# Optimization experiments

Measured on AMD Instinct MI355X. Metric: run time of the kernel, lower is better.

## Reference

```python
import jax, jax.numpy as jnp
import numpy as np

B, T, V, E, H = 512, 512, 50000, 100, 40


def gru_dir(x, lens, Wih, Whh, bih, bhh, reverse):
    """One GRU direction with length masking (PyTorch gate math).
    x: [B,T,I]; returns (out [B,T,H] zero-padded past lens, h_last [B,H])."""
    Bx, Tx, _ = x.shape
    Hh = Whh.shape[1]
    # precompute input-side gates: [T,B,3H]
    gx = jnp.einsum('bti,gi->tbg', x, Wih) + bih
    valid = (jnp.arange(Tx)[:, None] < lens[None, :])[..., None]  # [T,B,1]

    def step(h, inputs):
        gx_t, v = inputs
        gh = h @ Whh.T + bhh
        r = jax.nn.sigmoid(gx_t[:, :Hh] + gh[:, :Hh])
        z = jax.nn.sigmoid(gx_t[:, Hh:2 * Hh] + gh[:, Hh:2 * Hh])
        n = jnp.tanh(gx_t[:, 2 * Hh:] + r * gh[:, 2 * Hh:])
        hn = (1.0 - z) * n + z * h
        h = jnp.where(v, hn, h)          # freeze state past valid length
        return h, jnp.where(v, hn, 0.0)  # pad_packed_sequence zero-fills

    h0 = jnp.zeros((Bx, Hh), x.dtype)
    h_last, outs = jax.lax.scan(step, h0, (gx, valid), reverse=reverse)
    return jnp.transpose(outs, (1, 0, 2)), h_last


def setup_inputs() -> dict:
    key = jax.random.key(0)
    ks = jax.random.split(key, 24)
    text_len = jax.random.randint(ks[0], (B,), 1, T + 1)
    text = jax.random.randint(ks[1], (B, T), 1, V)
    text = jnp.where(jnp.arange(T)[None, :] < text_len[:, None], text, 0)
    s = 0.1
    emb = jax.random.normal(ks[2], (V, E), jnp.float32) * s
    emb = emb.at[0].set(0.0)  # padding_idx=0
    def mk(k, shape):
        return jax.random.normal(k, shape, jnp.float32) * s
    inp = {
        'text': text, 'text_len': text_len, 'emb': emb,
        'Wih0f': mk(ks[3], (3 * H, E)), 'Whh0f': mk(ks[4], (3 * H, H)),
        'bih0f': mk(ks[5], (3 * H,)), 'bhh0f': mk(ks[6], (3 * H,)),
        'Wih0b': mk(ks[7], (3 * H, E)), 'Whh0b': mk(ks[8], (3 * H, H)),
        'bih0b': mk(ks[9], (3 * H,)), 'bhh0b': mk(ks[10], (3 * H,)),
        'Wih1f': mk(ks[11], (3 * H, 2 * H)), 'Whh1f': mk(ks[12], (3 * H, H)),
        'bih1f': mk(ks[13], (3 * H,)), 'bhh1f': mk(ks[14], (3 * H,)),
        'Wih1b': mk(ks[15], (3 * H, 2 * H)), 'Whh1b': mk(ks[16], (3 * H, H)),
        'bih1b': mk(ks[17], (3 * H,)), 'bhh1b': mk(ks[18], (3 * H,)),
        'fc1_W': mk(ks[19], (128, 8 * H)), 'fc1_b': mk(ks[20], (128,)),
        'fc2_W': mk(ks[21], (1, 128)), 'fc2_b': mk(ks[22], (1,)),
    }
    return inp


def forward(text, text_len, emb, Wih0f, Whh0f, bih0f, bhh0f, Wih0b, Whh0b, bih0b, bhh0b,
            Wih1f, Whh1f, bih1f, bhh1f, Wih1b, Whh1b, bih1b, bhh1b,
            fc1_W, fc1_b, fc2_W, fc2_b):
    x = emb[text]  # [B,T,E]
    # layer 0 (bidirectional)
    of0, hf0 = gru_dir(x, text_len, Wih0f, Whh0f, bih0f, bhh0f, False)
    ob0, hb0 = gru_dir(x, text_len, Wih0b, Whh0b, bih0b, bhh0b, True)
    x1 = jnp.concatenate([of0, ob0], axis=-1)  # [B,T,2H]; inter-layer dropout is eval no-op
    # layer 1 (bidirectional)
    of1, hf1 = gru_dir(x1, text_len, Wih1f, Whh1f, bih1f, bhh1f, False)
    ob1, hb1 = gru_dir(x1, text_len, Wih1b, Whh1b, bih1b, bhh1b, True)
    out = jnp.concatenate([of1, ob1], axis=-1)  # [B,T,2H], zero past lens
    # masked avg / max pooling over valid timesteps
    avg_pool = jnp.sum(out, axis=1) / text_len[:, None].astype(out.dtype)
    valid = (jnp.arange(T)[None, :] < text_len[:, None])[..., None]  # [B,T,1]
    max_pool = jnp.max(jnp.where(valid, out, -jnp.inf), axis=1)
    # hidden order: [l0_fwd, l0_bwd, l1_fwd, l1_bwd]; cat([-1],[-2],[-3],[-4],...)
    pool_cat = jnp.concatenate([hb1, hf1, hb0, hf0, avg_pool, max_pool], axis=1)  # [B,8H]
    h = pool_cat @ fc1_W.T + fc1_b
    h = jnp.where(h >= 0, h, 0.01 * h)  # leaky_relu (dropouts are eval no-ops)
    return h @ fc2_W.T + fc2_b  # [B,1]


def reference(text, text_len, emb, Wih0f, Whh0f, bih0f, bhh0f, Wih0b, Whh0b, bih0b, bhh0b,
              Wih1f, Whh1f, bih1f, bhh1f, Wih1b, Whh1b, bih1b, bhh1b,
              fc1_W, fc1_b, fc2_W, fc2_b):
    return forward(text, text_len, emb, Wih0f, Whh0f, bih0f, bhh0f, Wih0b, Whh0b, bih0b, bhh0b,
                   Wih1f, Whh1f, bih1f, bhh1f, Wih1b, Whh1b, bih1b, bhh1b,
                   fc1_W, fc1_b, fc2_W, fc2_b)
```

## Files before the change

### kernel.cpp

```cpp
#include <hip/hip_runtime.h>
#include <hip/hip_fp16.h>

#define BB 512
#define TT 512
#define EE 100
#define HH 40
#define GG 120
#define TC 256
#define NC 2
#define NT (TC/64)
#define X1S 96
#define GXS 160

typedef _Float16 h2_t __attribute__((ext_vector_type(2)));
typedef _Float16 h8_t __attribute__((ext_vector_type(8)));
typedef float    f4_t __attribute__((ext_vector_type(4)));

__device__ __forceinline__ float fdot2_(h2_t a, h2_t b, float c) {
    return __builtin_amdgcn_fdot2(a, b, c, false);
}
__device__ __forceinline__ h2_t pack2_(float x, float y) {
    h2_t r; r[0] = (_Float16)x; r[1] = (_Float16)y; return r;
}
__device__ __forceinline__ float sigmoid_(float x) {
    return __builtin_amdgcn_rcpf(1.0f + __expf(-x));
}
__device__ __forceinline__ float tanhfast_(float x) {
    return 1.0f - 2.0f * __builtin_amdgcn_rcpf(__expf(2.0f * x) + 1.0f);
}

template<int K, bool GATHER>
__global__ __launch_bounds__(256, 1) void fused_kernel(
    const int cg, const int cs, const int nScan,
    const int* __restrict__ text, const __half* __restrict__ emb16,
    const __half* __restrict__ Xh,
    const _Float16* __restrict__ Wt,
    const float* __restrict__ bf, const float* __restrict__ bb,
    __half* __restrict__ gxW, const __half* __restrict__ gxR,
    const _Float16* __restrict__ WhhL,
    const float* __restrict__ bhhF, const float* __restrict__ bhhB,
    const int* __restrict__ lens,
    __half* __restrict__ out0,
    float* __restrict__ hcar, float* __restrict__ hlast,
    float* __restrict__ sumb, float* __restrict__ maxb)
{
    constexpr int KS = (K == 100) ? 4 : 3;
    const int tid = threadIdx.x;

    if ((int)blockIdx.x < nScan) {
        __builtin_amdgcn_s_setprio(3);
        const int wave = tid >> 6, j = tid & 63;
        if (j >= HH) return;
        const int chain = blockIdx.x * 4 + wave;
        const int dir = chain >> 9;
        const int b   = chain & (BB - 1);
        const float* bhh = dir ? bhhB : bhhF;

        h8_t R0,R1,R2,R3,R4, Z0,Z1,Z2,Z3,Z4, N0,N1,N2,N3,N4;
        {
            const _Float16* wr = WhhL + (size_t)dir * 4800;
            const h8_t* pr = (const h8_t*)(wr + (size_t)j * 40);
            const h8_t* pz = (const h8_t*)(wr + (size_t)(40 + j) * 40);
            const h8_t* pn = (const h8_t*)(wr + (size_t)(80 + j) * 40);
            R0=pr[0]; R1=pr[1]; R2=pr[2]; R3=pr[3]; R4=pr[4];
            Z0=pz[0]; Z1=pz[1]; Z2=pz[2]; Z3=pz[3]; Z4=pz[4];
            N0=pn[0]; N1=pn[1]; N2=pn[2]; N3=pn[3]; N4=pn[4];
        }
        asm volatile("" : "+v"(R0),"+v"(R1),"+v"(R2),"+v"(R3),"+v"(R4),
                          "+v"(Z0),"+v"(Z1),"+v"(Z2),"+v"(Z3),"+v"(Z4),
                          "+v"(N0),"+v"(N1),"+v"(N2),"+v"(N3),"+v"(N4));
        const float br = bhh[j], bz = bhh[HH + j], bn = bhh[2*HH + j];
        const int len = lens[b];
        const int chunk = dir ? (NC - 1 - cs) : cs;
        const int tbase = chunk * TC;

        int sBeg, sEnd;
        if (dir == 0) { sBeg = 0; sEnd = min(TC, max(0, len - tbase)); }
        else          { sBeg = max(0, tbase + TC - len); sEnd = TC; }

        float h = (cs == 0) ? 0.0f : hcar[(size_t)(dir * BB + b) * HH + j];
        float psum = 0.0f, pmax = -3.4e38f;
        const size_t gxRow = ((size_t)dir * BB + b) * TC;

        h2_t H0{},H1{},H2{},H3{},H4{},H5{},H6{},H7{},H8{},H9{},
             H10{},H11{},H12{},H13{},H14{},H15{},H16{},H17{},H18{},H19{};
#define RDL(L) __builtin_bit_cast(h2_t, __builtin_amdgcn_readlane(pk_, (L)))
#define REFRESH_H(val) do { \
        const int v_ = (int)__builtin_bit_cast(unsigned short, (_Float16)(val)); \
        const int t_ = __builtin_amdgcn_update_dpp(0, v_, 0x101, 0xf, 0xf, true); \
        const int pk_ = (t_ << 16) | (v_ & 0xffff); \
        H0=RDL(0);  H1=RDL(2);  H2=RDL(4);  H3=RDL(6);  H4=RDL(8); \
        H5=RDL(10); H6=RDL(12); H7=RDL(14); H8=RDL(16); H9=RDL(18); \
        H10=RDL(20); H11=RDL(22); H12=RDL(24); H13=RDL(26); H14=RDL(28); \
        H15=RDL(30); H16=RDL(32); H17=RDL(34); H18=RDL(36); H19=RDL(38); \
} while (0)
        REFRESH_H(h);

        struct G3 { __half r, z, n; };
        auto ldg3 = [&](int sc) -> G3 {
            const int scc = max(0, min(sc, sEnd - 1));
            const int tl = dir ? (TC - 1 - scc) : scc;
            const uint2 v = *(const uint2*)(gxR + (gxRow + tl) * GXS + j * 4);
            G3 g;
            g.r = __builtin_bit_cast(__half, (unsigned short)(v.x & 0xffff));
            g.z = __builtin_bit_cast(__half, (unsigned short)(v.x >> 16));
            g.n = __builtin_bit_cast(__half, (unsigned short)(v.y & 0xffff));
            return g;
        };
#define SL(V,i) __builtin_shufflevector(V, V, 2*(i), 2*(i)+1)
#define DOTQ(Rq,Zq,Nq, A,B,C,D) \
        r0 = fdot2_(SL(Rq,0), (A), r0); \
        z0 = fdot2_(SL(Zq,0), (A), z0); \
        n0 = fdot2_(SL(Nq,0), (A), n0); \
        r1 = fdot2_(SL(Rq,1), (B), r1); \
        z1 = fdot2_(SL(Zq,1), (B), z1); \
        n1 = fdot2_(SL(Nq,1), (B), n1); \
        r0 = fdot2_(SL(Rq,2), (C), r0); \
        z0 = fdot2_(SL(Zq,2), (C), z0); \
        n0 = fdot2_(SL(Nq,2), (C), n0); \
        r1 = fdot2_(SL(Rq,3), (D), r1); \
        z1 = fdot2_(SL(Zq,3), (D), z1); \
        n1 = fdot2_(SL(Nq,3), (D), n1);

        constexpr int PF = 4;
        auto step = [&](int s, G3& g, bool pf) {
            G3 nx;
            if (pf) nx = ldg3(s + PF);
            const int tloc = dir ? (TC - 1 - s) : s;
            float r0 = br, r1 = 0.f, z0 = bz, z1 = 0.f, n0 = bn, n1 = 0.f;
            DOTQ(R0,Z0,N0, H0,H1,H2,H3)
            DOTQ(R1,Z1,N1, H4,H5,H6,H7)
            DOTQ(R2,Z2,N2, H8,H9,H10,H11)
            DOTQ(R3,Z3,N3, H12,H13,H14,H15)
            DOTQ(R4,Z4,N4, H16,H17,H18,H19)
            const float rr = sigmoid_(__half2float(g.r) + r0 + r1);
            const float zz = sigmoid_(__half2float(g.z) + z0 + z1);
            const float nn = tanhfast_(__half2float(g.n) + rr * (n0 + n1));
            const float hn = (1.0f - zz) * nn + zz * h;
            h = hn;
            REFRESH_H(hn);
            if (GATHER) {
                const int t = tbase + tloc;
                out0[((size_t)b * TT + t) * X1S + dir*HH + j] = __float2half(hn);
            } else {
                psum += hn;
                pmax = fmaxf(pmax, hn);
            }
            if (pf) g = nx;
        };

        G3 q0 = {}, q1 = {}, q2 = {}, q3 = {};
        if (sBeg < sEnd) {
            q0 = ldg3(sBeg);
            q1 = ldg3(sBeg + 1);
            q2 = ldg3(sBeg + 2);
            q3 = ldg3(sBeg + 3);
        }
        int s = sBeg;
        for (; s + PF <= sEnd; s += PF) {
            step(s + 0, q0, true);
            step(s + 1, q1, true);
            step(s + 2, q2, true);
            step(s + 3, q3, true);
        }
        if (s     < sEnd) step(s,     q0, false);
        if (s + 1 < sEnd) step(s + 1, q1, false);
        if (s + 2 < sEnd) step(s + 2, q2, false);

        hcar[(size_t)(dir * BB + b) * HH + j] = h;
        const int layer = GATHER ? 0 : 1;
        if (cs == NC - 1)
            hlast[((size_t)(layer * 2 + dir) * BB + b) * HH + j] = h;
        if (!GATHER) {
            const size_t pi = (size_t)b * (2*HH) + dir*HH + j;
            if (cs == 0) { sumb[pi] = psum;  maxb[pi] = pmax; }
            else         { sumb[pi] += psum; maxb[pi] = fmaxf(maxb[pi], pmax); }
        }
        return;
    }

    __builtin_amdgcn_s_setprio(0);
    const int gid = blockIdx.x - nScan;
    const int b    = gid & (BB - 1);
    const int tile = (gid >> 9) & (NT - 1);
    const int dir  = gid >> (9 + 2);
    const int chunk = dir ? (NC - 1 - cg) : cg;
    const int tbase = chunk * TC + tile * 64;
    if (tbase >= lens[b]) return;
    const float* bias = dir ? bb : bf;
    const _Float16* Wg = Wt + (size_t)dir * (KS * 8 * 64 * 8);

    const int w = tid >> 6, l = tid & 63;
    const int row = l & 15, kq = l >> 4;
    const int t0 = tbase + w * 16 + row;
    h8_t A[4];
    if (GATHER) {
        const int tok = text[b * TT + t0];
        const _Float16* ap = (const _Float16*)emb16 + (size_t)tok * 128 + kq * 8;
        #pragma unroll
        for (int ks = 0; ks < KS; ++ks) A[ks] = *(const h8_t*)(ap + ks * 32);
    } else {
        const _Float16* ap = (const _Float16*)Xh + ((size_t)b * TT + t0) * X1S + kq * 8;
        #pragma unroll
        for (int ks = 0; ks < KS; ++ks) A[ks] = *(const h8_t*)(ap + ks * 32);
    }

    f4_t acc[8] = {};
    #pragma unroll
    for (int ks = 0; ks < KS; ++ks)
        #pragma unroll
        for (int f = 0; f < 8; ++f) {
            const h8_t Bf = *(const h8_t*)(Wg + ((size_t)(ks * 8 + f) * 64 + l) * 8);
            acc[f] = __builtin_amdgcn_mfma_f32_16x16x32_f16(A[ks], Bf, acc[f], 0, 0, 0);
        }

    const size_t rowB = ((size_t)dir * BB + b) * TC;
    const int gb = l & 15, rq = l >> 4;
    #pragma unroll
    for (int f = 0; f < 8; ++f) {
        const int gate = f * 16 + gb;
        if (gate < GG) {
            const int jj   = (gate >= 80) ? (gate - 80) : (gate >= 40 ? gate - 40 : gate);
            const int slot = (gate >= 80) ? 2 : (gate >= 40 ? 1 : 0);
            const float bv = bias[gate];
            #pragma unroll
            for (int r = 0; r < 4; ++r) {
                const int tloc = tile * 64 + w * 16 + rq * 4 + r;
                gxW[(rowB + tloc) * GXS + jj * 4 + slot] = __float2half(acc[f][r] + bv);
            }
        }
    }
}

#define NE2 (50000 * 64)
#define NW0 (2*4*8*64)
#define NW1 (2*3*8*64)
#define NHH (4*120*20)
#define NP0 (BB*TT*8)
__global__ __launch_bounds__(256) void prep_kernel(
    const float* __restrict__ emb,
    const float* __restrict__ Wih0f, const float* __restrict__ Wih0b,
    const float* __restrict__ Wih1f, const float* __restrict__ Wih1b,
    const float* __restrict__ Whh0f, const float* __restrict__ Whh0b,
    const float* __restrict__ Whh1f, const float* __restrict__ Whh1b,
    __half* __restrict__ emb16, _Float16* __restrict__ Wt16,
    _Float16* __restrict__ Whh16, __half* __restrict__ out0)
{
    const int gid = blockIdx.x * 256 + threadIdx.x;
    if (gid < NE2) {
        const int v = gid >> 6, q2 = gid & 63;
        const int k0 = q2 * 2;
        float x0 = 0.f, x1 = 0.f;
        if (k0 < EE) { x0 = emb[(size_t)v * EE + k0]; x1 = emb[(size_t)v * EE + k0 + 1]; }
        ((h2_t*)emb16)[(size_t)v * 64 + q2] = pack2_(x0, x1);
        return;
    }
    int e = gid - NE2;
    if (e < NP0) {
        const int row = e >> 3, q = e & 7;
        ((h2_t*)out0)[(size_t)row * 48 + 40 + q] = pack2_(0.f, 0.f);
        return;
    }
    e -= NP0;
    if (e < NW0) {
        const int l = e & 63, f = (e >> 6) & 7, ks = (e >> 9) & 3, dir = e >> 11;
        const float* W = dir ? Wih0b : Wih0f;
        const int col = f * 16 + (l & 15);
        const int kb  = ks * 32 + (l >> 4) * 8;
        _Float16* dst = Wt16 + (size_t)e * 8;
        #pragma unroll
        for (int i = 0; i < 8; ++i) {
            const int k = kb + i;
            dst[i] = (_Float16)((col < GG && k < EE) ? W[(size_t)col * EE + k] : 0.f);
        }
        return;
    }
    e -= NW0;
    if (e < NW1) {
        const int l = e & 63, f = (e >> 6) & 7;
        const int t = e >> 9;
        const int ks = t % 3, dir = t / 3;
        const float* W = dir ? Wih1b : Wih1f;
        const int col = f * 16 + (l & 15);
        const int kb  = ks * 32 + (l >> 4) * 8;
        _Float16* dst = Wt16 + (size_t)(NW0 + e) * 8;
        #pragma unroll
        for (int i = 0; i < 8; ++i) {
            const int k = kb + i;
            dst[i] = (_Float16)((col < GG && k < 2*HH) ? W[(size_t)col * (2*HH) + k] : 0.f);
        }
        return;
    }
    e -= NW1;
    if (e < NHH) {
        const int ld = e / 2400, rem = e - ld * 2400;
        const int row2 = rem / 20, kk = rem - row2 * 20;
        const float* W = (ld == 0) ? Whh0f : (ld == 1) ? Whh0b
                       : (ld == 2) ? Whh1f : Whh1b;
        ((h2_t*)Whh16)[e] = pack2_(W[row2*HH + 2*kk], W[row2*HH + 2*kk + 1]);
    }
}

__global__ __launch_bounds__(128) void fc_kernel(
    const float* __restrict__ hlast, const float* __restrict__ sumb,
    const float* __restrict__ maxb, const int* __restrict__ lens,
    const float* __restrict__ fc1W, const float* __restrict__ fc1b,
    const float* __restrict__ fc2W, const float* __restrict__ fc2b,
    float* __restrict__ out)
{
    __shared__ float pool[8 * HH];
    __shared__ float red[128];
    const int b = blockIdx.x, tid = threadIdx.x;
    if (tid < HH) {
        pool[tid]        = hlast[(size_t)(3*BB + b) * HH + tid];
        pool[HH + tid]   = hlast[(size_t)(2*BB + b) * HH + tid];
        pool[2*HH + tid] = hlast[(size_t)(1*BB + b) * HH + tid];
        pool[3*HH + tid] = hlast[(size_t)(0*BB + b) * HH + tid];
    }
    const float invLen = 1.0f / (float)lens[b];
    if (tid < 2*HH) {
        pool[4*HH + tid] = sumb[(size_t)b * 2*HH + tid] * invLen;
        pool[6*HH + tid] = maxb[(size_t)b * 2*HH + tid];
    }
    __syncthreads();
    float acc = fc1b[tid];
    for (int k = 0; k < 8*HH; ++k)
        acc = fmaf(pool[k], fc1W[(size_t)tid * (8*HH) + k], acc);
    float v = (acc >= 0.0f) ? acc : 0.01f * acc;
    red[tid] = v * fc2W[tid];
    __syncthreads();
    for (int s = 64; s > 0; s >>= 1) {
        if (tid < s) red[tid] += red[tid + s];
        __syncthreads();
    }
    if (tid == 0) out[b] = red[0] + fc2b[0];
}

extern "C" void kernel_launch(void* const* d_in, const int* in_sizes, int n_in,
                              void* d_out, int out_size, void* d_ws, size_t ws_size,
                              hipStream_t stream) {
    const int*   text  = (const int*)d_in[0];
    const int*   lens  = (const int*)d_in[1];
    const float* emb   = (const float*)d_in[2];
    const float* Wih0f = (const float*)d_in[3];
    const float* Whh0f = (const float*)d_in[4];
    const float* bih0f = (const float*)d_in[5];
    const float* bhh0f = (const float*)d_in[6];
    const float* Wih0b = (const float*)d_in[7];
    const float* Whh0b = (const float*)d_in[8];
    const float* bih0b = (const float*)d_in[9];
    const float* bhh0b = (const float*)d_in[10];
    const float* Wih1f = (const float*)d_in[11];
    const float* Whh1f = (const float*)d_in[12];
    const float* bih1f = (const float*)d_in[13];
    const float* bhh1f = (const float*)d_in[14];
    const float* Wih1b = (const float*)d_in[15];
    const float* Whh1b = (const float*)d_in[16];
    const float* bih1b = (const float*)d_in[17];
    const float* bhh1b = (const float*)d_in[18];
    const float* fc1W  = (const float*)d_in[19];
    const float* fc1b  = (const float*)d_in[20];
    const float* fc2W  = (const float*)d_in[21];
    const float* fc2b  = (const float*)d_in[22];
    float* out = (float*)d_out;

    char* p = (char*)d_ws;
    const size_t gxB = (size_t)2 * BB * TC * GXS * sizeof(__half);
    __half* gxb0  = (__half*)p;  p += gxB;
    __half* gxb1  = (__half*)p;  p += gxB;
    __half* out0  = (__half*)p;  p += (size_t)BB * TT * X1S * sizeof(__half);
    float*  hcar  = (float*)p;   p += (size_t)2 * BB * HH * sizeof(float);
    float*  hlast = (float*)p;   p += (size_t)4 * BB * HH * sizeof(float);
    float*  sumb  = (float*)p;   p += (size_t)BB * 2 * HH * sizeof(float);
    float*  maxb  = (float*)p;   p += (size_t)BB * 2 * HH * sizeof(float);
    __half*    emb16 = (__half*)p;    p += (size_t)50000 * 128 * sizeof(__half);
    _Float16*  Wt16  = (_Float16*)p;  p += (size_t)(NW0 + NW1) * 8 * sizeof(_Float16);
    _Float16*  Whh16 = (_Float16*)p;
    __half* gxb[2] = { gxb0, gxb1 };

    const int NG = BB * 2 * NT;
    const int NS = 256;

    {
        const int total = NE2 + NP0 + NW0 + NW1 + NHH;
        prep_kernel<<<(total + 255) / 256, 256, 0, stream>>>(
            emb, Wih0f, Wih0b, Wih1f, Wih1b, Whh0f, Whh0b, Whh1f, Whh1b,
            emb16, Wt16, Whh16, out0);
    }

    fused_kernel<EE, true><<<NG, 256, 0, stream>>>(0, 0, 0,
        text, emb16, nullptr, Wt16, bih0f, bih0b,
        gxb[0], gxb[0], Whh16, bhh0f, bhh0b,
        lens, out0, hcar, hlast, sumb, maxb);
    for (int ci = 1; ci < NC; ++ci)
        fused_kernel<EE, true><<<NS + NG, 256, 0, stream>>>(ci, ci - 1, NS,
            text, emb16, nullptr, Wt16, bih0f, bih0b,
            gxb[ci & 1], gxb[(ci - 1) & 1], Whh16, bhh0f, bhh0b,
            lens, out0, hcar, hlast, sumb, maxb);
    fused_kernel<EE, true><<<NS, 256, 0, stream>>>(0, NC - 1, NS,
        text, emb16, nullptr, Wt16, bih0f, bih0b,
        gxb[0], gxb[(NC - 1) & 1], Whh16, bhh0f, bhh0b,
        lens, out0, hcar, hlast, sumb, maxb);

    fused_kernel<2*HH, false><<<NG, 256, 0, stream>>>(0, 0, 0,
        text, emb16, out0, Wt16 + (size_t)NW0 * 8, bih1f, bih1b,
        gxb[0], gxb[0], Whh16 + 9600, bhh1f, bhh1b,
        lens, out0, hcar, hlast, sumb, maxb);
    for (int ci = 1; ci < NC; ++ci)
        fused_kernel<2*HH, false><<<NS + NG, 256, 0, stream>>>(ci, ci - 1, NS,
            text, emb16, out0, Wt16 + (size_t)NW0 * 8, bih1f, bih1b,
            gxb[ci & 1], gxb[(ci - 1) & 1], Whh16 + 9600, bhh1f, bhh1b,
            lens, out0, hcar, hlast, sumb, maxb);
    fused_kernel<2*HH, false><<<NS, 256, 0, stream>>>(0, NC - 1, NS,
        text, emb16, out0, Wt16 + (size_t)NW0 * 8, bih1f, bih1b,
        gxb[0], gxb[(NC - 1) & 1], Whh16 + 9600, bhh1f, bhh1b,
        lens, out0, hcar, hlast, sumb, maxb);

    fc_kernel<<<BB, 128, 0, stream>>>(hlast, sumb, maxb, lens,
        fc1W, fc1b, fc2W, fc2b, out);
}
```

Before: 506.3 us.

## Double-buffer input-gate loads in 16-step windows for the GRU scan

Replaces the rolling 4-step register prefetch of precomputed input gates with two 16-entry register buffers. The next 16-step window is loaded while the current one is processed. The aim is to hide global-memory latency behind the serial recurrence by issuing many loads in a batch. The extra buffers raise VGPR pressure, and the per-step bounds checks inside the unrolled windows add branching at partial windows.

```diff
diff --git a/kernel.cpp b/kernel.cpp
--- a/kernel.cpp
+++ b/kernel.cpp
@@ -96,17 +96,6 @@
 } while (0)
         REFRESH_H(h);
 
-        struct G3 { __half r, z, n; };
-        auto ldg3 = [&](int sc) -> G3 {
-            const int scc = max(0, min(sc, sEnd - 1));
-            const int tl = dir ? (TC - 1 - scc) : scc;
-            const uint2 v = *(const uint2*)(gxR + (gxRow + tl) * GXS + j * 4);
-            G3 g;
-            g.r = __builtin_bit_cast(__half, (unsigned short)(v.x & 0xffff));
-            g.z = __builtin_bit_cast(__half, (unsigned short)(v.x >> 16));
-            g.n = __builtin_bit_cast(__half, (unsigned short)(v.y & 0xffff));
-            return g;
-        };
 #define SL(V,i) __builtin_shufflevector(V, V, 2*(i), 2*(i)+1)
 #define DOTQ(Rq,Zq,Nq, A,B,C,D) \
         r0 = fdot2_(SL(Rq,0), (A), r0); \
@@ -122,50 +111,58 @@
         z1 = fdot2_(SL(Zq,3), (D), z1); \
         n1 = fdot2_(SL(Nq,3), (D), n1);
 
-        constexpr int PF = 4;
-        auto step = [&](int s, G3& g, bool pf) {
-            G3 nx;
-            if (pf) nx = ldg3(s + PF);
-            const int tloc = dir ? (TC - 1 - s) : s;
+        auto body = [&](int s, uint2 v) {
+            const __half gr = __builtin_bit_cast(__half, (unsigned short)(v.x & 0xffff));
+            const __half gz = __builtin_bit_cast(__half, (unsigned short)(v.x >> 16));
+            const __half gn = __builtin_bit_cast(__half, (unsigned short)(v.y & 0xffff));
             float r0 = br, r1 = 0.f, z0 = bz, z1 = 0.f, n0 = bn, n1 = 0.f;
             DOTQ(R0,Z0,N0, H0,H1,H2,H3)
             DOTQ(R1,Z1,N1, H4,H5,H6,H7)
             DOTQ(R2,Z2,N2, H8,H9,H10,H11)
             DOTQ(R3,Z3,N3, H12,H13,H14,H15)
             DOTQ(R4,Z4,N4, H16,H17,H18,H19)
-            const float rr = sigmoid_(__half2float(g.r) + r0 + r1);
-            const float zz = sigmoid_(__half2float(g.z) + z0 + z1);
-            const float nn = tanhfast_(__half2float(g.n) + rr * (n0 + n1));
+            const float rr = sigmoid_(__half2float(gr) + r0 + r1);
+            const float zz = sigmoid_(__half2float(gz) + z0 + z1);
+            const float nn = tanhfast_(__half2float(gn) + rr * (n0 + n1));
             const float hn = (1.0f - zz) * nn + zz * h;
             h = hn;
             REFRESH_H(hn);
             if (GATHER) {
-                const int t = tbase + tloc;
-                out0[((size_t)b * TT + t) * X1S + dir*HH + j] = __float2half(hn);
+                const int tloc = dir ? (TC - 1 - s) : s;
+                out0[((size_t)b * TT + tbase + tloc) * X1S + dir*HH + j] =
+                    __float2half(hn);
             } else {
                 psum += hn;
                 pmax = fmaxf(pmax, hn);
             }
-            if (pf) g = nx;
         };
 
-        G3 q0 = {}, q1 = {}, q2 = {}, q3 = {};
+        uint2 GA[16], GB[16];
+#define LDW(W, G) do { _Pragma("unroll") \
+        for (int k_ = 0; k_ < 16; ++k_) { \
+            const int sc_ = max(0, min((W) * 16 + k_, sEnd - 1)); \
+            const int tl_ = dir ? (TC - 1 - sc_) : sc_; \
+            G[k_] = *(const uint2*)(gxR + (gxRow + tl_) * GXS + j * 4); \
+        } } while (0)
+#define RUNW(W, G) do { _Pragma("unroll") \
+        for (int k_ = 0; k_ < 16; ++k_) { \
+            const int s_ = (W) * 16 + k_; \
+            if (s_ >= sBeg && s_ < sEnd) body(s_, G[k_]); \
+        } } while (0)
+
         if (sBeg < sEnd) {
-            q0 = ldg3(sBeg);
-            q1 = ldg3(sBeg + 1);
-            q2 = ldg3(sBeg + 2);
-            q3 = ldg3(sBeg + 3);
-        }
-        int s = sBeg;
-        for (; s + PF <= sEnd; s += PF) {
-            step(s + 0, q0, true);
-            step(s + 1, q1, true);
-            step(s + 2, q2, true);
-            step(s + 3, q3, true);
-        }
-        if (s     < sEnd) step(s,     q0, false);
-        if (s + 1 < sEnd) step(s + 1, q1, false);
-        if (s + 2 < sEnd) step(s + 2, q2, false);
+            const int W0 = sBeg >> 4, W1 = (sEnd - 1) >> 4;
+            LDW(W0, GA);
+            for (int W = W0; W <= W1; ++W) {
+                if (((W - W0) & 1) == 0) {
+                    if (W < W1) LDW(W + 1, GB);
+                    RUNW(W, GA);
+                } else {
+                    if (W < W1) LDW(W + 1, GA);
+                    RUNW(W, GB);
+                }
+            }
+        }
 
         hcar[(size_t)(dir * BB + b) * HH + j] = h;
         const int layer = GATHER ? 0 : 1;
```

New measurement: 609.1 us. 20.3% more time.
